# Kernel optimization log

Measured on AMD Instinct MI355X. Metric: run time of the kernel, lower is better.

Reference implementation:

```python
import jax, jax.numpy as jnp
import numpy as np

HIDDEN = 2048
N_HEADS = 16
HEAD_DIM = 128
N_EXPERTS = 8
TOP_K = 2
INTER = 1024
EPS = 1e-5
ROPE_THETA = 10000.0
T = 2048


def rms_norm(x, w, eps=EPS):
    xf = x.astype(jnp.float32)
    return (xf * jax.lax.rsqrt(jnp.mean(xf * xf, axis=-1, keepdims=True) + eps)).astype(x.dtype) * w


def apply_rope(x, positions):
    # x: [T, H, D], NeoX-style half rotation
    d = x.shape[-1]
    inv_freq = 1.0 / (ROPE_THETA ** (jnp.arange(0, d, 2, dtype=jnp.float32) / d))
    ang = positions.astype(jnp.float32)[:, None] * inv_freq  # [T, D/2]
    cos = jnp.cos(ang)[:, None, :]
    sin = jnp.sin(ang)[:, None, :]
    x1, x2 = jnp.split(x, 2, axis=-1)
    return jnp.concatenate([x1 * cos - x2 * sin, x2 * cos + x1 * sin], axis=-1)


def setup_inputs() -> dict:
    key = jax.random.key(0)
    ks = jax.random.split(key, 8)
    s = 0.02
    return {
        "positions": jnp.arange(T, dtype=jnp.int32),
        "hidden_states": jax.random.normal(ks[0], (T, HIDDEN), jnp.float32),
        "qkv_w": jax.random.normal(ks[1], (3 * HIDDEN, HIDDEN), jnp.float32) * s,
        "o_w": jax.random.normal(ks[2], (HIDDEN, HIDDEN), jnp.float32) * s,
        "q_norm_w": jnp.ones((N_HEADS * HEAD_DIM,), jnp.float32),
        "k_norm_w": jnp.ones((N_HEADS * HEAD_DIM,), jnp.float32),
        "post_attn_norm_w": jnp.ones((HIDDEN,), jnp.float32),
        "post_ffn_norm_w": jnp.ones((HIDDEN,), jnp.float32),
        "gate_w": jax.random.normal(ks[3], (N_EXPERTS, HIDDEN), jnp.float32) * s,
        "w_gate": jax.random.normal(ks[4], (N_EXPERTS, INTER, HIDDEN), jnp.float32) * s,
        "w_up": jax.random.normal(ks[5], (N_EXPERTS, INTER, HIDDEN), jnp.float32) * s,
        "w_down": jax.random.normal(ks[6], (N_EXPERTS, HIDDEN, INTER), jnp.float32) * s,
    }


def attention(positions, x, qkv_w, o_w, q_norm_w, k_norm_w):
    qkv = x @ qkv_w.T  # [T, 3*HIDDEN]
    q, k, v = jnp.split(qkv, 3, axis=-1)
    q = rms_norm(q, q_norm_w)  # norm over full flat q dim (FlexOlmo/OLMoE style)
    k = rms_norm(k, k_norm_w)
    q = apply_rope(q.reshape(T, N_HEADS, HEAD_DIM), positions)
    k = apply_rope(k.reshape(T, N_HEADS, HEAD_DIM), positions)
    v = v.reshape(T, N_HEADS, HEAD_DIM)
    scale = 1.0 / np.sqrt(HEAD_DIM)
    scores = jnp.einsum('thd,shd->hts', q, k) * scale
    mask = jnp.tril(jnp.ones((T, T), bool))
    scores = jnp.where(mask[None], scores, -jnp.inf)
    p = jax.nn.softmax(scores, axis=-1)
    out = jnp.einsum('hts,shd->thd', p, v).reshape(T, HIDDEN)
    return out @ o_w.T


def moe(x, gate_w, w_gate, w_up, w_down):
    logits = (x @ gate_w.T).astype(jnp.float32)  # router_logits.float()
    probs = jax.nn.softmax(logits, axis=-1)
    topv, topi = jax.lax.top_k(probs, TOP_K)  # renormalize=False -> use raw softmax weights
    # dense per-expert combine weights: [T, E]
    wdense = jnp.zeros((T, N_EXPERTS), jnp.float32)
    wdense = jnp.sum(jax.nn.one_hot(topi, N_EXPERTS, dtype=jnp.float32) * topv[..., None], axis=1)
    # detach().clone() before dispatch (inference semantics: value unchanged)
    xe = jax.lax.stop_gradient(x)
    g = jnp.einsum('td,efd->tef', xe, w_gate)
    u = jnp.einsum('td,efd->tef', xe, w_up)
    h = jax.nn.silu(g) * u
    y = jnp.einsum('tef,edf->ted', h, w_down)
    return jnp.einsum('ted,te->td', y, wdense)


def reference(positions, hidden_states, qkv_w, o_w, q_norm_w, k_norm_w,
              post_attn_norm_w, post_ffn_norm_w, gate_w, w_gate, w_up, w_down):
    residual = hidden_states
    h = attention(positions, hidden_states, qkv_w, o_w, q_norm_w, k_norm_w)
    h = rms_norm(h, post_attn_norm_w)
    h = h + residual
    residual = h
    h = moe(h, gate_w, w_gate, w_up, w_down)
    h = rms_norm(h, post_ffn_norm_w)
    return residual + h
```

## Files before the change

### kernel.cpp

```cpp
#include <hip/hip_runtime.h>
#include <hip/hip_bf16.h>
#include <cmath>

#define TT 2048
#define HID 2048
#define NHEADS 16
#define HDIM 128
#define NEXP 8
#define INTERD 1024
#define EPSV 1e-5f

typedef short bf16x8 __attribute__((ext_vector_type(8)));
typedef float f32x4 __attribute__((ext_vector_type(4)));

__device__ __forceinline__ unsigned short f2bf(float f) {
    unsigned int u = __builtin_bit_cast(unsigned int, f);
    unsigned int r = (u + 0x7FFFu + ((u >> 16) & 1u)) >> 16;
    return (unsigned short)r;
}
__device__ __forceinline__ float bf2f(unsigned short h) {
    return __builtin_bit_cast(float, (unsigned int)h << 16);
}

__device__ __forceinline__ void gll16(const void* g, void* l) {
    __builtin_amdgcn_global_load_lds((const __attribute__((address_space(1))) void*)g,
                                     (__attribute__((address_space(3))) void*)l, 16, 0, 0);
}

__device__ __forceinline__ float block_reduce_sum_256(float v, float* red) {
    const int tid = threadIdx.x;
    red[tid] = v;
    __syncthreads();
    for (int s = 128; s > 0; s >>= 1) {
        if (tid < s) red[tid] += red[tid + s];
        __syncthreads();
    }
    float r = red[0];
    __syncthreads();
    return r;
}

__global__ __launch_bounds__(256) void split_f32k(const float* __restrict__ x,
                                                  unsigned short* __restrict__ hi,
                                                  unsigned short* __restrict__ lo, int n4) {
    int i = blockIdx.x * 256 + threadIdx.x;
    if (i >= n4) return;
    float4 v = reinterpret_cast<const float4*>(x)[i];
    float xs[4] = {v.x, v.y, v.z, v.w};
    unsigned short hs[4], ls[4];
#pragma unroll
    for (int u = 0; u < 4; ++u) {
        hs[u] = f2bf(xs[u]);
        ls[u] = f2bf(xs[u] - bf2f(hs[u]));
    }
    uint2 hp; hp.x = hs[0] | ((unsigned)hs[1] << 16); hp.y = hs[2] | ((unsigned)hs[3] << 16);
    uint2 lp; lp.x = ls[0] | ((unsigned)ls[1] << 16); lp.y = ls[2] | ((unsigned)ls[3] << 16);
    *reinterpret_cast<uint2*>(hi + (size_t)i * 4) = hp;
    *reinterpret_cast<uint2*>(lo + (size_t)i * 4) = lp;
}

#define GSTAGE(BUF, K0)                                                             \
    {                                                                               \
        char* base_ = (char*)Smem + (BUF) * 32768;                                  \
        _Pragma("unroll")                                                           \
        for (int i_ = 0; i_ < 2; ++i_) {                                            \
            int c_ = tid + i_ * 256;                                                \
            int r_ = c_ >> 2, s_ = c_ & 3;                                          \
            int ko_ = (K0) + (((s_ ^ (r_ & 3)) & 3) << 3);                          \
            gll16(Ah + (size_t)(m0 + r_) * lda + ko_, base_ + c_ * 16);             \
            gll16(Al + (size_t)(m0 + r_) * lda + ko_, base_ + 8192 + c_ * 16);      \
            gll16(Bh + (size_t)(n0 + r_) * K + ko_, base_ + 16384 + c_ * 16);       \
            gll16(Bl + (size_t)(n0 + r_) * K + ko_, base_ + 24576 + c_ * 16);       \
        }                                                                           \
    }

__global__ __launch_bounds__(256) void gemm_sp(const unsigned short* __restrict__ Ah,
                                               const unsigned short* __restrict__ Al,
                                               const unsigned short* __restrict__ Bh,
                                               const unsigned short* __restrict__ Bl,
                                               float* __restrict__ C, int N, int K, int lda) {
    const int nbx = gridDim.x;
    const int nwg = nbx * gridDim.y;
    const int orig = blockIdx.y * nbx + blockIdx.x;
    const int qq = nwg >> 3, rr = nwg & 7;
    const int xcd = orig & 7, loc = orig >> 3;
    const int wgid = (xcd < rr ? xcd * (qq + 1) : rr * (qq + 1) + (xcd - rr) * qq) + loc;
    const int m0 = (wgid / nbx) * 128, n0 = (wgid % nbx) * 128;

    __shared__ __align__(16) unsigned short Smem[2 * 4 * 128 * 32];
    const int tid = threadIdx.x;
    const int w = tid >> 6, l = tid & 63;
    const int lr = l & 15, lg = l >> 4;
    const int wm = w >> 1, wn = w & 1;

    f32x4 acc[4][4];
#pragma unroll
    for (int i = 0; i < 4; ++i)
#pragma unroll
        for (int j = 0; j < 4; ++j) acc[i][j] = f32x4{0.f, 0.f, 0.f, 0.f};

    const int nks = K >> 5;
    GSTAGE(0, 0);
    int cur = 0;
    for (int ks = 0; ks < nks; ++ks) {
        if (ks + 1 < nks) {
            GSTAGE(cur ^ 1, (ks + 1) << 5);
            asm volatile("s_waitcnt vmcnt(8)" ::: "memory");
        } else {
            asm volatile("s_waitcnt vmcnt(0)" ::: "memory");
        }
        __builtin_amdgcn_s_barrier();
        __builtin_amdgcn_sched_barrier(0);
        char* bb = (char*)Smem + cur * 32768;
        bf16x8 bhf[4], blf[4];
#pragma unroll
        for (int nt = 0; nt < 4; ++nt) {
            int row = wn * 64 + nt * 16 + lr;
            int off = row * 64 + (((lg ^ (row & 3)) & 3) << 4);
            bhf[nt] = *reinterpret_cast<const bf16x8*>(bb + 16384 + off);
            blf[nt] = *reinterpret_cast<const bf16x8*>(bb + 24576 + off);
        }
        __builtin_amdgcn_s_setprio(1);
#pragma unroll
        for (int mt = 0; mt < 4; ++mt) {
            int row = wm * 64 + mt * 16 + lr;
            int off = row * 64 + (((lg ^ (row & 3)) & 3) << 4);
            bf16x8 ahf = *reinterpret_cast<const bf16x8*>(bb + off);
            bf16x8 alf = *reinterpret_cast<const bf16x8*>(bb + 8192 + off);
#pragma unroll
            for (int nt = 0; nt < 4; ++nt) {
                acc[mt][nt] = __builtin_amdgcn_mfma_f32_16x16x32_bf16(ahf, bhf[nt], acc[mt][nt], 0, 0, 0);
                acc[mt][nt] = __builtin_amdgcn_mfma_f32_16x16x32_bf16(ahf, blf[nt], acc[mt][nt], 0, 0, 0);
                acc[mt][nt] = __builtin_amdgcn_mfma_f32_16x16x32_bf16(alf, bhf[nt], acc[mt][nt], 0, 0, 0);
            }
        }
        __builtin_amdgcn_s_setprio(0);
        asm volatile("s_waitcnt lgkmcnt(0)" ::: "memory");
        __builtin_amdgcn_s_barrier();
        __builtin_amdgcn_sched_barrier(0);
        cur ^= 1;
    }
#pragma unroll
    for (int mt = 0; mt < 4; ++mt) {
#pragma unroll
        for (int r = 0; r < 4; ++r) {
            size_t crow = (size_t)(m0 + wm * 64 + mt * 16 + lg * 4 + r) * N;
#pragma unroll
            for (int nt = 0; nt < 4; ++nt)
                C[crow + n0 + wn * 64 + nt * 16 + lr] = acc[mt][nt][r];
        }
    }
}

template<int ABF, int MODE>
__global__ __launch_bounds__(256) void gemm_moe(const void* __restrict__ Ap,
                                                const float* __restrict__ B,
                                                float* __restrict__ C,
                                                const float* __restrict__ gsrc,
                                                int N, int K, int lda,
                                                size_t strideB,
                                                const int* __restrict__ gather,
                                                const int* __restrict__ offs,
                                                const int* __restrict__ counts) {
    const int e = blockIdx.z;
    const int cnt = counts[e];
    const int base = offs[e];
    const int m0 = blockIdx.y * 128;
    if (m0 >= cnt) return;
    const int n0 = blockIdx.x * 128;
    const float* Bp = B + (size_t)e * strideB;

    __shared__ unsigned short smA[128 * 64];
    __shared__ unsigned short smB[128 * 64];
    __shared__ int rowsA[128];
    const int tid = threadIdx.x;
    if (tid < 128) {
        int rr = min(m0 + tid, cnt - 1);
        rowsA[tid] = gather ? gather[base + rr] : (base + rr);
    }
    __syncthreads();

    const int w = tid >> 6, l = tid & 63;
    const int lr = l & 15, lg = l >> 4;
    const int wm = w >> 1, wn = w & 1;
    char* sA = (char*)smA;
    char* sB = (char*)smB;

    f32x4 acc[4][4];
#pragma unroll
    for (int i = 0; i < 4; ++i)
#pragma unroll
        for (int j = 0; j < 4; ++j) acc[i][j] = f32x4{0.f, 0.f, 0.f, 0.f};

    for (int k0 = 0; k0 < K; k0 += 64) {
        if (ABF) {
            const unsigned short* Abf = (const unsigned short*)Ap;
#pragma unroll
            for (int i = 0; i < 4; ++i) {
                int slot = tid + i * 256;
                int r = slot >> 3, sg = slot & 7;
                uint4 v = *reinterpret_cast<const uint4*>(&Abf[(size_t)rowsA[r] * lda + k0 + sg * 8]);
                *reinterpret_cast<uint4*>(sA + r * 128 + ((sg * 16) ^ ((r & 7) << 4))) = v;
            }
        } else {
            const float* Af = (const float*)Ap;
#pragma unroll
            for (int i = 0; i < 8; ++i) {
                int slot = tid + i * 256;
                int r = slot >> 4, kq = slot & 15;
                float4 av = *reinterpret_cast<const float4*>(&Af[(size_t)rowsA[r] * lda + k0 + kq * 4]);
                uint2 pk;
                pk.x = (unsigned)f2bf(av.x) | ((unsigned)f2bf(av.y) << 16);
                pk.y = (unsigned)f2bf(av.z) | ((unsigned)f2bf(av.w) << 16);
                *reinterpret_cast<uint2*>(sA + r * 128 + ((kq * 8) ^ ((r & 7) << 4))) = pk;
            }
        }
#pragma unroll
        for (int i = 0; i < 8; ++i) {
            int slot = tid + i * 256;
            int r = slot >> 4, kq = slot & 15;
            float4 bv = *reinterpret_cast<const float4*>(&Bp[(size_t)(n0 + r) * K + k0 + kq * 4]);
            uint2 pk;
            pk.x = (unsigned)f2bf(bv.x) | ((unsigned)f2bf(bv.y) << 16);
            pk.y = (unsigned)f2bf(bv.z) | ((unsigned)f2bf(bv.w) << 16);
            *reinterpret_cast<uint2*>(sB + r * 128 + ((kq * 8) ^ ((r & 7) << 4))) = pk;
        }
        __syncthreads();
#pragma unroll
        for (int kk = 0; kk < 2; ++kk) {
            bf16x8 af[4], bfr[4];
#pragma unroll
            for (int mt = 0; mt < 4; ++mt) {
                int row = wm * 64 + mt * 16 + lr;
                af[mt] = *reinterpret_cast<const bf16x8*>(sA + row * 128 + ((kk * 64 + lg * 16) ^ ((row & 7) << 4)));
            }
#pragma unroll
            for (int nt = 0; nt < 4; ++nt) {
                int row = wn * 64 + nt * 16 + lr;
                bfr[nt] = *reinterpret_cast<const bf16x8*>(sB + row * 128 + ((kk * 64 + lg * 16) ^ ((row & 7) << 4)));
            }
#pragma unroll
            for (int mt = 0; mt < 4; ++mt)
#pragma unroll
                for (int nt = 0; nt < 4; ++nt)
                    acc[mt][nt] = __builtin_amdgcn_mfma_f32_16x16x32_bf16(af[mt], bfr[nt], acc[mt][nt], 0, 0, 0);
        }
        __syncthreads();
    }
#pragma unroll
    for (int mt = 0; mt < 4; ++mt) {
#pragma unroll
        for (int r = 0; r < 4; ++r) {
            int rowl = wm * 64 + mt * 16 + lg * 4 + r;
            if (m0 + rowl < cnt) {
                size_t crow = (size_t)(base + m0 + rowl) * N;
#pragma unroll
                for (int nt = 0; nt < 4; ++nt) {
                    size_t idx = crow + n0 + wn * 64 + nt * 16 + lr;
                    if (MODE == 1) {
                        float g = gsrc[idx];
                        C[idx] = g / (1.f + expf(-g)) * acc[mt][nt][r];
                    } else {
                        C[idx] = acc[mt][nt][r];
                    }
                }
            }
        }
    }
}

__global__ __launch_bounds__(256) void qknorm_rope_split(float* __restrict__ qkv,
                                                         const float* __restrict__ qw,
                                                         const float* __restrict__ kw,
                                                         const int* __restrict__ pos) {
    __shared__ float xbuf[2048];
    __shared__ float red[256];
    const int t = blockIdx.x, tid = threadIdx.x;
    unsigned short* row16 = (unsigned short*)(qkv + (size_t)t * 6144);
    const float pf = (float)pos[t];
    float vreg[8];
    const float* vsrc = qkv + (size_t)t * 6144 + 4096;
#pragma unroll
    for (int i = 0; i < 8; ++i) vreg[i] = vsrc[tid + i * 256];
    __syncthreads();
#pragma unroll
    for (int i = 0; i < 8; ++i) {
        int d = tid + i * 256;
        unsigned short hi = f2bf(vreg[i]);
        row16[8192 + d] = hi;
        row16[10240 + d] = f2bf(vreg[i] - bf2f(hi));
    }
    for (int part = 0; part < 2; ++part) {
        const float* x = qkv + (size_t)t * 6144 + part * 2048;
        const float* wn = part ? kw : qw;
        const int sbase = part ? 4096 : 0;
        const float outscale = part ? 1.0f : 0.08838834764831845f;
        float s = 0.f;
#pragma unroll
        for (int i = 0; i < 8; ++i) {
            int d = tid + i * 256;
            float v = x[d];
            xbuf[d] = v;
            s = fmaf(v, v, s);
        }
        float tot = block_reduce_sum_256(s, red);
        float scale = rsqrtf(tot * (1.f / HID) + EPSV);
#pragma unroll
        for (int p = tid; p < 1024; p += 256) {
            int hh = p >> 6, j = p & 63;
            int i1 = hh * 128 + j, i2 = i1 + 64;
            float x1 = xbuf[i1] * scale * wn[i1];
            float x2 = xbuf[i2] * scale * wn[i2];
            float invf = expf(-(float)j * 0.14391156831212787f);
            float ang = pf * invf;
            float sn, cs;
            sincosf(ang, &sn, &cs);
            float o1 = (x1 * cs - x2 * sn) * outscale;
            float o2 = (x2 * cs + x1 * sn) * outscale;
            unsigned short h1_ = f2bf(o1);
            row16[sbase + i1] = h1_;
            row16[sbase + 2048 + i1] = f2bf(o1 - bf2f(h1_));
            unsigned short h2_ = f2bf(o2);
            row16[sbase + i2] = h2_;
            row16[sbase + 2048 + i2] = f2bf(o2 - bf2f(h2_));
        }
        __syncthreads();
    }
}

__global__ __launch_bounds__(256) void kvprep(const unsigned short* __restrict__ qkv16,
                                              unsigned short* __restrict__ kt,
                                              unsigned short* __restrict__ vt) {
    const int C = blockIdx.x;
    const int h = blockIdx.y;
    const int tid = threadIdx.x;
#pragma unroll
    for (int p = 0; p < 2; ++p) {
#pragma unroll
        for (int i = 0; i < 4; ++i) {
            int slot = tid + i * 256;
            int r = slot >> 4, sg = slot & 15;
            uint4 v = *reinterpret_cast<const uint4*>(
                qkv16 + (size_t)(C * 64 + r) * 12288 + 4096 + p * 2048 + h * 128 + (sg ^ (r & 7)) * 8);
            *reinterpret_cast<uint4*>(kt + (size_t)(h * 32 + C) * 16384 + p * 8192 + slot * 8) = v;
        }
    }
    __shared__ unsigned short tile[64 * 128];
    char* tb = (char*)tile;
    for (int p = 0; p < 2; ++p) {
#pragma unroll
        for (int i = 0; i < 4; ++i) {
            int c = tid + i * 256;
            int r = c >> 4, dseg = c & 15;
            uint4 v = *reinterpret_cast<const uint4*>(
                qkv16 + (size_t)(C * 64 + r) * 12288 + 8192 + p * 2048 + h * 128 + dseg * 8);
            int swz = dseg ^ (r & 7) ^ (r >> 3);
            *reinterpret_cast<uint4*>(tb + r * 256 + swz * 16) = v;
        }
        __syncthreads();
        unsigned short* ob = vt + (size_t)(h * 32 + C) * 16384 + p * 8192;
#pragma unroll
        for (int i = 0; i < 4; ++i) {
            int c = tid + i * 256;
            int d = c >> 3, j = c & 7;
            unsigned short tmp[8];
#pragma unroll
            for (int u = 0; u < 8; ++u) {
                int s = 8 * j + u;
                int swz = (d >> 3) ^ (s & 7) ^ (s >> 3);
                tmp[u] = *reinterpret_cast<const unsigned short*>(tb + s * 256 + swz * 16 + (d & 7) * 2);
            }
            *reinterpret_cast<uint4*>(ob + (size_t)d * 64 + ((j ^ (d & 7)) * 8)) =
                *reinterpret_cast<const uint4*>(tmp);
        }
        __syncthreads();
    }
}

#define STAGE1(CIDX)                                                                   \
    {                                                                                  \
        const unsigned short* kb_ = kt + (size_t)(h * 32 + (CIDX)) * 16384;            \
        const unsigned short* vb_ = vt + (size_t)(h * 32 + (CIDX)) * 16384;            \
        _Pragma("unroll")                                                              \
        for (int p_ = 0; p_ < 2; ++p_) {                                               \
            _Pragma("unroll")                                                          \
            for (int i_ = 0; i_ < 4; ++i_) {                                           \
                int slot_ = tid + i_ * 256;                                            \
                gll16(kb_ + p_ * 8192 + slot_ * 8, kvb + p_ * 16384 + slot_ * 16);     \
                gll16(vb_ + p_ * 8192 + slot_ * 8, kvb + 32768 + p_ * 16384 + slot_ * 16); \
            }                                                                          \
        }                                                                              \
    }

__global__ __launch_bounds__(256) void attn_mfma(const unsigned short* __restrict__ qkv16,
                                                 const unsigned short* __restrict__ kt,
                                                 const unsigned short* __restrict__ vt,
                                                 unsigned short* __restrict__ oh,
                                                 unsigned short* __restrict__ ol) {
    const int g = blockIdx.x;
    const int rank = (g < 256) ? g : 767 - g;
    const int h = rank & 15;
    const int t0 = (31 - (rank >> 4)) * 64;
    const int tid = threadIdx.x;
    const int w = tid >> 6, l = tid & 63;
    const int lr = l & 15, lg = l >> 4;
    const size_t RS = 12288;
    __shared__ __align__(16) unsigned short KVs[32768];
    __shared__ unsigned short Ps[4][2 * 16 * 64];
    char* kvb = (char*)KVs;
    char* PsB = (char*)(Ps[w]);

    bf16x8 qh[4], ql[4];
    {
        const unsigned short* qp = qkv16 + (size_t)(t0 + w * 16 + lr) * RS + h * 128 + lg * 8;
#pragma unroll
        for (int kk = 0; kk < 4; ++kk) {
            qh[kk] = *reinterpret_cast<const bf16x8*>(qp + kk * 32);
            ql[kk] = *reinterpret_cast<const bf16x8*>(qp + 2048 + kk * 32);
        }
    }
    f32x4 oacc[8];
#pragma unroll
    for (int dt = 0; dt < 8; ++dt) oacc[dt] = f32x4{0.f, 0.f, 0.f, 0.f};
    float mrun[4] = {-INFINITY, -INFINITY, -INFINITY, -INFINITY};
    float lrun[4] = {0.f, 0.f, 0.f, 0.f};

    for (int s0 = 0; s0 <= t0; s0 += 64) {
        STAGE1(s0 >> 6);
        __syncthreads();
        char* KsB = kvb;
        char* VtB = kvb + 32768;

        f32x4 sc[4];
#pragma unroll
        for (int nt = 0; nt < 4; ++nt) sc[nt] = f32x4{0.f, 0.f, 0.f, 0.f};
        __builtin_amdgcn_s_setprio(1);
#pragma unroll
        for (int kk = 0; kk < 4; ++kk) {
#pragma unroll
            for (int nt = 0; nt < 4; ++nt) {
                int row = nt * 16 + lr;
                int off = row * 256 + ((kk * 64 + lg * 16) ^ ((row & 7) << 4));
                bf16x8 kh = *reinterpret_cast<const bf16x8*>(KsB + off);
                bf16x8 kl = *reinterpret_cast<const bf16x8*>(KsB + 16384 + off);
                sc[nt] = __builtin_amdgcn_mfma_f32_16x16x32_bf16(qh[kk], kh, sc[nt], 0, 0, 0);
                sc[nt] = __builtin_amdgcn_mfma_f32_16x16x32_bf16(ql[kk], kh, sc[nt], 0, 0, 0);
                sc[nt] = __builtin_amdgcn_mfma_f32_16x16x32_bf16(qh[kk], kl, sc[nt], 0, 0, 0);
            }
        }
        __builtin_amdgcn_s_setprio(0);
        float mnew[4], alpha[4], psum[4];
#pragma unroll
        for (int r = 0; r < 4; ++r) {
            int row_t = t0 + w * 16 + lg * 4 + r;
            float mx = mrun[r];
#pragma unroll
            for (int nt = 0; nt < 4; ++nt) {
                int col = s0 + nt * 16 + lr;
                float v = sc[nt][r];
                if (col > row_t) v = -INFINITY;
                sc[nt][r] = v;
                mx = fmaxf(mx, v);
            }
#pragma unroll
            for (int o = 1; o < 16; o <<= 1) mx = fmaxf(mx, __shfl_xor(mx, o));
            mnew[r] = mx;
            alpha[r] = expf(mrun[r] - mx);
            mrun[r] = mx;
            psum[r] = 0.f;
        }
#pragma unroll
        for (int nt = 0; nt < 4; ++nt) {
#pragma unroll
            for (int r = 0; r < 4; ++r) {
                float p = expf(sc[nt][r] - mnew[r]);
                psum[r] += p;
                int prow = lg * 4 + r;
                int off = prow * 128 + (((nt * 16 + lr) * 2) ^ ((prow & 7) << 4));
                unsigned short ph = f2bf(p);
                *reinterpret_cast<unsigned short*>(PsB + off) = ph;
                *reinterpret_cast<unsigned short*>(PsB + 2048 + off) = f2bf(p - bf2f(ph));
            }
        }
#pragma unroll
        for (int r = 0; r < 4; ++r) {
            float s = psum[r];
#pragma unroll
            for (int o = 1; o < 16; o <<= 1) s += __shfl_xor(s, o);
            lrun[r] = lrun[r] * alpha[r] + s;
        }
#pragma unroll
        for (int dt = 0; dt < 8; ++dt)
#pragma unroll
            for (int r = 0; r < 4; ++r) oacc[dt][r] *= alpha[r];
        bf16x8 ph[2], pl[2];
#pragma unroll
        for (int kk = 0; kk < 2; ++kk) {
            int off = lr * 128 + ((kk * 64 + lg * 16) ^ ((lr & 7) << 4));
            ph[kk] = *reinterpret_cast<const bf16x8*>(PsB + off);
            pl[kk] = *reinterpret_cast<const bf16x8*>(PsB + 2048 + off);
        }
        __builtin_amdgcn_s_setprio(1);
#pragma unroll
        for (int dt = 0; dt < 8; ++dt) {
            int row = dt * 16 + lr;
#pragma unroll
            for (int kk = 0; kk < 2; ++kk) {
                int off = row * 128 + ((kk * 64 + lg * 16) ^ ((row & 7) << 4));
                bf16x8 vh = *reinterpret_cast<const bf16x8*>(VtB + off);
                bf16x8 vl = *reinterpret_cast<const bf16x8*>(VtB + 16384 + off);
                oacc[dt] = __builtin_amdgcn_mfma_f32_16x16x32_bf16(ph[kk], vh, oacc[dt], 0, 0, 0);
                oacc[dt] = __builtin_amdgcn_mfma_f32_16x16x32_bf16(ph[kk], vl, oacc[dt], 0, 0, 0);
                oacc[dt] = __builtin_amdgcn_mfma_f32_16x16x32_bf16(pl[kk], vh, oacc[dt], 0, 0, 0);
            }
        }
        __builtin_amdgcn_s_setprio(0);
        __syncthreads();
    }
#pragma unroll
    for (int r = 0; r < 4; ++r) {
        float inv = 1.f / lrun[r];
        int row_t = t0 + w * 16 + lg * 4 + r;
#pragma unroll
        for (int dt = 0; dt < 8; ++dt) {
            float o = oacc[dt][r] * inv;
            unsigned short hb = f2bf(o);
            size_t idx = (size_t)row_t * 2048 + h * 128 + dt * 16 + lr;
            oh[idx] = hb;
            ol[idx] = f2bf(o - bf2f(hb));
        }
    }
}

__global__ __launch_bounds__(256) void add_rmsnorm(const float* __restrict__ resid,
                                                   const float* __restrict__ x,
                                                   const float* __restrict__ w,
                                                   float* __restrict__ out,
                                                   unsigned short* __restrict__ outbf) {
    __shared__ float red[256];
    const int t = blockIdx.x, tid = threadIdx.x;
    const float* xr = x + (size_t)t * HID;
    float v[8];
    float s = 0.f;
#pragma unroll
    for (int i = 0; i < 8; ++i) { v[i] = xr[tid + i * 256]; s = fmaf(v[i], v[i], s); }
    float tot = block_reduce_sum_256(s, red);
    float scale = rsqrtf(tot * (1.f / HID) + EPSV);
#pragma unroll
    for (int i = 0; i < 8; ++i) {
        int d = tid + i * 256;
        float o = resid[(size_t)t * HID + d] + v[i] * scale * w[d];
        out[(size_t)t * HID + d] = o;
        outbf[(size_t)t * HID + d] = f2bf(o);
    }
}

__global__ __launch_bounds__(64) void router_kernel(const float* __restrict__ h1,
                                                    const float* __restrict__ gate_w,
                                                    int* __restrict__ topi, float* __restrict__ topv,
                                                    int* __restrict__ slot_tk, int* __restrict__ counts) {
    const int t = blockIdx.x, lane = threadIdx.x;
    float acc[NEXP] = {};
    const float* x = h1 + (size_t)t * HID;
    for (int d = lane; d < HID; d += 64) {
        float xv = x[d];
#pragma unroll
        for (int e = 0; e < NEXP; ++e) acc[e] = fmaf(xv, gate_w[e * HID + d], acc[e]);
    }
#pragma unroll
    for (int e = 0; e < NEXP; ++e)
#pragma unroll
        for (int off = 32; off > 0; off >>= 1) acc[e] += __shfl_down(acc[e], off);
    if (lane == 0) {
        float mx = acc[0];
        for (int e = 1; e < NEXP; ++e) mx = fmaxf(mx, acc[e]);
        float p[NEXP], se = 0.f;
        for (int e = 0; e < NEXP; ++e) { p[e] = expf(acc[e] - mx); se += p[e]; }
        float inv = 1.f / se;
        for (int e = 0; e < NEXP; ++e) p[e] *= inv;
        int e1 = 0;
        for (int e = 1; e < NEXP; ++e) if (p[e] > p[e1]) e1 = e;
        int e2 = (e1 == 0) ? 1 : 0;
        for (int e = 0; e < NEXP; ++e) if (e != e1 && p[e] > p[e2]) e2 = e;
        topi[t * 2] = e1;     topv[t * 2] = p[e1];
        topi[t * 2 + 1] = e2; topv[t * 2 + 1] = p[e2];
        slot_tk[t * 2]     = atomicAdd(&counts[e1], 1);
        slot_tk[t * 2 + 1] = atomicAdd(&counts[e2], 1);
    }
}

__global__ void scan_kernel(const int* __restrict__ counts, int* __restrict__ offs) {
    int o = 0;
    for (int e = 0; e < NEXP; ++e) { offs[e] = o; o += counts[e]; }
}

__global__ __launch_bounds__(256) void map_kernel(const int* __restrict__ topi,
                                                  const int* __restrict__ slot_tk,
                                                  const int* __restrict__ offs,
                                                  int* __restrict__ token_of_row,
                                                  int* __restrict__ row_of_tk) {
    int idx = blockIdx.x * 256 + threadIdx.x;
    if (idx >= TT * 2) return;
    int e = topi[idx];
    int row = offs[e] + slot_tk[idx];
    token_of_row[row] = idx >> 1;
    row_of_tk[idx] = row;
}

__global__ __launch_bounds__(256) void final_combine(const float* __restrict__ h1,
                                                     const float* __restrict__ ypart,
                                                     const float* __restrict__ topv,
                                                     const int* __restrict__ row_of_tk,
                                                     const float* __restrict__ wffn,
                                                     float* __restrict__ out) {
    __shared__ float red[256];
    const int t = blockIdx.x, tid = threadIdx.x;
    const int r0 = row_of_tk[t * 2], r1 = row_of_tk[t * 2 + 1];
    const float w0 = topv[t * 2], w1 = topv[t * 2 + 1];
    const float* y0 = ypart + (size_t)r0 * HID;
    const float* y1 = ypart + (size_t)r1 * HID;
    float v[8];
    float s = 0.f;
#pragma unroll
    for (int i = 0; i < 8; ++i) {
        int d = tid + i * 256;
        v[i] = w0 * y0[d] + w1 * y1[d];
        s = fmaf(v[i], v[i], s);
    }
    float tot = block_reduce_sum_256(s, red);
    float scale = rsqrtf(tot * (1.f / HID) + EPSV);
#pragma unroll
    for (int i = 0; i < 8; ++i) {
        int d = tid + i * 256;
        out[(size_t)t * HID + d] = h1[(size_t)t * HID + d] + v[i] * scale * wffn[d];
    }
}

extern "C" void kernel_launch(void* const* d_in, const int* in_sizes, int n_in,
                              void* d_out, int out_size, void* d_ws, size_t ws_size,
                              hipStream_t stream) {
    const int*   positions = (const int*)d_in[0];
    const float* hidden    = (const float*)d_in[1];
    const float* qkv_w     = (const float*)d_in[2];
    const float* o_w       = (const float*)d_in[3];
    const float* q_norm_w  = (const float*)d_in[4];
    const float* k_norm_w  = (const float*)d_in[5];
    const float* post_attn = (const float*)d_in[6];
    const float* post_ffn  = (const float*)d_in[7];
    const float* gate_w    = (const float*)d_in[8];
    const float* w_gate    = (const float*)d_in[9];
    const float* w_up      = (const float*)d_in[10];
    const float* w_down    = (const float*)d_in[11];
    float* out = (float*)d_out;

    char* ws = (char*)d_ws;
    size_t off = 0;
    auto alloc = [&](size_t bytes) -> void* {
        void* p = ws + off;
        off += (bytes + 255) & ~(size_t)255;
        return p;
    };
    float*          qkvbuf = (float*)alloc((size_t)TT * 6144 * 4);
    unsigned short* hidsp  = (unsigned short*)alloc((size_t)TT * HID * 2 * 2);
    unsigned short* wsp    = (unsigned short*)alloc(((size_t)6144 * HID * 2 + (size_t)HID * HID * 2) * 2);
    float*          h1     = (float*)alloc((size_t)TT * HID * 4);
    unsigned short* h1bf   = (unsigned short*)alloc((size_t)TT * HID * 2);
    int*   topi   = (int*)alloc(TT * 2 * 4);
    float* topv   = (float*)alloc(TT * 2 * 4);
    int*   slot   = (int*)alloc(TT * 2 * 4);
    int*   rowtk  = (int*)alloc(TT * 2 * 4);
    int*   tokrow = (int*)alloc(TT * 2 * 4);
    int*   counts = (int*)alloc(8 * 4);
    int*   offsb  = (int*)alloc(8 * 4);
    if (off > ws_size) return;

    unsigned short* hid_hi   = hidsp;
    unsigned short* hid_lo   = hidsp + (size_t)TT * HID;
    unsigned short* attnO_hi = hid_hi;
    unsigned short* attnO_lo = hid_lo;
    unsigned short* qkvw_hi = wsp;
    unsigned short* qkvw_lo = wsp + (size_t)6144 * HID;
    unsigned short* ow_hi   = wsp + (size_t)2 * 6144 * HID;
    unsigned short* ow_lo   = ow_hi + (size_t)HID * HID;
    unsigned short* vtbuf   = wsp;
    unsigned short* ktbuf   = wsp + (size_t)TT * HID * 2;
    float* gbuf   = qkvbuf;
    float* hinter = qkvbuf + (size_t)4096 * INTERD;
    float* oOut   = qkvbuf + (size_t)8192 * INTERD;
    float* ypart  = oOut;

    hipMemsetAsync(counts, 0, 8 * sizeof(int), stream);

    dim3 b256(256);
    split_f32k<<<dim3(TT * HID / 4 / 256), b256, 0, stream>>>(hidden, hid_hi, hid_lo, TT * HID / 4);
    split_f32k<<<dim3(6144 * HID / 4 / 256), b256, 0, stream>>>(qkv_w, qkvw_hi, qkvw_lo, 6144 * HID / 4);
    split_f32k<<<dim3(HID * HID / 4 / 256), b256, 0, stream>>>(o_w, ow_hi, ow_lo, HID * HID / 4);
    gemm_sp<<<dim3(6144 / 128, TT / 128), b256, 0, stream>>>(hid_hi, hid_lo, qkvw_hi, qkvw_lo,
                                                             qkvbuf, 6144, HID, HID);
    qknorm_rope_split<<<dim3(TT), b256, 0, stream>>>(qkvbuf, q_norm_w, k_norm_w, positions);
    kvprep<<<dim3(32, NHEADS), b256, 0, stream>>>((const unsigned short*)qkvbuf, ktbuf, vtbuf);
    attn_mfma<<<dim3(512), b256, 0, stream>>>((const unsigned short*)qkvbuf, ktbuf, vtbuf,
                                              attnO_hi, attnO_lo);
    gemm_sp<<<dim3(HID / 128, TT / 128), b256, 0, stream>>>(attnO_hi, attnO_lo, ow_hi, ow_lo,
                                                            oOut, HID, HID, HID);
    add_rmsnorm<<<dim3(TT), b256, 0, stream>>>(hidden, oOut, post_attn, h1, h1bf);
    router_kernel<<<dim3(TT), dim3(64), 0, stream>>>(h1, gate_w, topi, topv, slot, counts);
    scan_kernel<<<1, 1, 0, stream>>>(counts, offsb);
    map_kernel<<<dim3((TT * 2 + 255) / 256), b256, 0, stream>>>(topi, slot, offsb, tokrow, rowtk);
    gemm_moe<1, 0><<<dim3(INTERD / 128, 32, NEXP), b256, 0, stream>>>(
        h1bf, w_gate, gbuf, nullptr, INTERD, HID, HID, (size_t)INTERD * HID, tokrow, offsb, counts);
    gemm_moe<1, 1><<<dim3(INTERD / 128, 32, NEXP), b256, 0, stream>>>(
        h1bf, w_up, hinter, gbuf, INTERD, HID, HID, (size_t)INTERD * HID, tokrow, offsb, counts);
    gemm_moe<0, 0><<<dim3(HID / 128, 32, NEXP), b256, 0, stream>>>(
        hinter, w_down, ypart, nullptr, HID, INTERD, INTERD, (size_t)HID * INTERD, nullptr, offsb, counts);
    final_combine<<<dim3(TT), b256, 0, stream>>>(h1, ypart, topv, rowtk, post_ffn, out);
}
```

Baseline: 696.7 us.

## Pre-convert MoE gate/up weights to bf16 and use async-LDS pipelined expert GEMM

Adds a conversion kernel that turns the fp32 w_gate and w_up expert weights into bf16 buffers in the workspace. The gate and up GEMMs then use a new double-buffered kernel with direct global-to-LDS loads, instead of converting fp32 B tiles inside the loop. The up GEMM now writes the SiLU-gated intermediate as bf16, so the down GEMM reads bf16 A directly. The LDS swizzle also changes to XOR with (row>>1)&3 to reduce bank conflicts. The risk is the extra weight-conversion traffic on every call, plus lower precision in the intermediate.

```diff
diff --git a/kernel.cpp b/kernel.cpp
--- a/kernel.cpp
+++ b/kernel.cpp
@@ -59,6 +59,17 @@
     *reinterpret_cast<uint2*>(lo + (size_t)i * 4) = lp;
 }
 
+__global__ __launch_bounds__(256) void cvt_bf(const float* __restrict__ x,
+                                              unsigned short* __restrict__ y, int n4) {
+    int i = blockIdx.x * 256 + threadIdx.x;
+    if (i >= n4) return;
+    float4 v = reinterpret_cast<const float4*>(x)[i];
+    uint2 p;
+    p.x = (unsigned)f2bf(v.x) | ((unsigned)f2bf(v.y) << 16);
+    p.y = (unsigned)f2bf(v.z) | ((unsigned)f2bf(v.w) << 16);
+    *reinterpret_cast<uint2*>(y + (size_t)i * 4) = p;
+}
+
 #define GSTAGE(BUF, K0)                                                             \
     {                                                                               \
         char* base_ = (char*)Smem + (BUF) * 32768;                                  \
@@ -66,7 +77,7 @@
         for (int i_ = 0; i_ < 2; ++i_) {                                            \
             int c_ = tid + i_ * 256;                                                \
             int r_ = c_ >> 2, s_ = c_ & 3;                                          \
-            int ko_ = (K0) + (((s_ ^ (r_ & 3)) & 3) << 3);                          \
+            int ko_ = (K0) + (((s_ ^ ((r_ >> 1) & 3)) & 3) << 3);                   \
             gll16(Ah + (size_t)(m0 + r_) * lda + ko_, base_ + c_ * 16);             \
             gll16(Al + (size_t)(m0 + r_) * lda + ko_, base_ + 8192 + c_ * 16);      \
             gll16(Bh + (size_t)(n0 + r_) * K + ko_, base_ + 16384 + c_ * 16);       \
@@ -116,7 +127,7 @@
 #pragma unroll
         for (int nt = 0; nt < 4; ++nt) {
             int row = wn * 64 + nt * 16 + lr;
-            int off = row * 64 + (((lg ^ (row & 3)) & 3) << 4);
+            int off = row * 64 + (((lg ^ ((row >> 1) & 3)) & 3) << 4);
             bhf[nt] = *reinterpret_cast<const bf16x8*>(bb + 16384 + off);
             blf[nt] = *reinterpret_cast<const bf16x8*>(bb + 24576 + off);
         }
@@ -124,7 +135,7 @@
 #pragma unroll
         for (int mt = 0; mt < 4; ++mt) {
             int row = wm * 64 + mt * 16 + lr;
-            int off = row * 64 + (((lg ^ (row & 3)) & 3) << 4);
+            int off = row * 64 + (((lg ^ ((row >> 1) & 3)) & 3) << 4);
             bf16x8 ahf = *reinterpret_cast<const bf16x8*>(bb + off);
             bf16x8 alf = *reinterpret_cast<const bf16x8*>(bb + 8192 + off);
 #pragma unroll
@@ -152,16 +163,120 @@
     }
 }
 
-template<int ABF, int MODE>
-__global__ __launch_bounds__(256) void gemm_moe(const void* __restrict__ Ap,
-                                                const float* __restrict__ B,
-                                                float* __restrict__ C,
-                                                const float* __restrict__ gsrc,
-                                                int N, int K, int lda,
-                                                size_t strideB,
-                                                const int* __restrict__ gather,
-                                                const int* __restrict__ offs,
-                                                const int* __restrict__ counts) {
+#define GSTAGE_BF(BUF, K0)                                                           \
+    {                                                                                \
+        char* base_ = sm + (BUF) * 16384;                                            \
+        int ko_ = (K0) + x0s;                                                        \
+        gll16(A + arow0 * lda + ko_, base_ + tid * 16);                              \
+        gll16(A + arow1 * lda + ko_, base_ + (tid + 256) * 16);                      \
+        gll16(Bp + brow0 * K + ko_, base_ + 8192 + tid * 16);                        \
+        gll16(Bp + brow1 * K + ko_, base_ + 8192 + (tid + 256) * 16);                \
+    }
+
+template<int MODE>
+__global__ __launch_bounds__(256) void gemm_bf(const unsigned short* __restrict__ A,
+                                               const unsigned short* __restrict__ B,
+                                               void* __restrict__ Cout,
+                                               const float* __restrict__ gsrc,
+                                               int N, int K, int lda,
+                                               size_t strideB,
+                                               const int* __restrict__ gather,
+                                               const int* __restrict__ offs,
+                                               const int* __restrict__ counts) {
+    const int e = blockIdx.z;
+    const int cnt = counts[e];
+    const int base = offs[e];
+    const int m0 = blockIdx.y * 128;
+    if (m0 >= cnt) return;
+    const int n0 = blockIdx.x * 128;
+    const unsigned short* Bp = B + (size_t)e * strideB;
+
+    __shared__ __align__(16) unsigned short Smem[2 * 2 * 128 * 32];
+    char* sm = (char*)Smem;
+    const int tid = threadIdx.x;
+    const int w = tid >> 6, l = tid & 63;
+    const int lr = l & 15, lg = l >> 4;
+    const int wm = w >> 1, wn = w & 1;
+
+    const int r0 = tid >> 2, s0 = tid & 3;
+    const int r1 = r0 + 64;
+    const int x0s = ((s0 ^ ((r0 >> 1) & 3)) & 3) << 3;
+    const size_t arow0 = (size_t)gather[base + min(m0 + r0, cnt - 1)];
+    const size_t arow1 = (size_t)gather[base + min(m0 + r1, cnt - 1)];
+    const size_t brow0 = (size_t)(n0 + r0);
+    const size_t brow1 = (size_t)(n0 + r1);
+
+    f32x4 acc[4][4];
+#pragma unroll
+    for (int i = 0; i < 4; ++i)
+#pragma unroll
+        for (int j = 0; j < 4; ++j) acc[i][j] = f32x4{0.f, 0.f, 0.f, 0.f};
+
+    const int nks = K >> 5;
+    GSTAGE_BF(0, 0);
+    int cur = 0;
+    for (int ks = 0; ks < nks; ++ks) {
+        if (ks + 1 < nks) {
+            GSTAGE_BF(cur ^ 1, (ks + 1) << 5);
+            asm volatile("s_waitcnt vmcnt(4)" ::: "memory");
+        } else {
+            asm volatile("s_waitcnt vmcnt(0)" ::: "memory");
+        }
+        __builtin_amdgcn_s_barrier();
+        __builtin_amdgcn_sched_barrier(0);
+        char* bb = sm + cur * 16384;
+        bf16x8 bfr[4];
+#pragma unroll
+        for (int nt = 0; nt < 4; ++nt) {
+            int row = wn * 64 + nt * 16 + lr;
+            int off = row * 64 + (((lg ^ ((row >> 1) & 3)) & 3) << 4);
+            bfr[nt] = *reinterpret_cast<const bf16x8*>(bb + 8192 + off);
+        }
+        __builtin_amdgcn_s_setprio(1);
+#pragma unroll
+        for (int mt = 0; mt < 4; ++mt) {
+            int row = wm * 64 + mt * 16 + lr;
+            int off = row * 64 + (((lg ^ ((row >> 1) & 3)) & 3) << 4);
+            bf16x8 af = *reinterpret_cast<const bf16x8*>(bb + off);
+#pragma unroll
+            for (int nt = 0; nt < 4; ++nt)
+                acc[mt][nt] = __builtin_amdgcn_mfma_f32_16x16x32_bf16(af, bfr[nt], acc[mt][nt], 0, 0, 0);
+        }
+        __builtin_amdgcn_s_setprio(0);
+        asm volatile("s_waitcnt lgkmcnt(0)" ::: "memory");
+        __builtin_amdgcn_s_barrier();
+        __builtin_amdgcn_sched_barrier(0);
+        cur ^= 1;
+    }
+#pragma unroll
+    for (int mt = 0; mt < 4; ++mt) {
+#pragma unroll
+        for (int r = 0; r < 4; ++r) {
+            int rowl = wm * 64 + mt * 16 + lg * 4 + r;
+            if (m0 + rowl < cnt) {
+                size_t crow = (size_t)(base + m0 + rowl) * N;
+#pragma unroll
+                for (int nt = 0; nt < 4; ++nt) {
+                    size_t idx = crow + n0 + wn * 64 + nt * 16 + lr;
+                    if (MODE == 1) {
+                        float g = gsrc[idx];
+                        ((unsigned short*)Cout)[idx] = f2bf(g / (1.f + expf(-g)) * acc[mt][nt][r]);
+                    } else {
+                        ((float*)Cout)[idx] = acc[mt][nt][r];
+                    }
+                }
+            }
+        }
+    }
+}
+
+__global__ __launch_bounds__(256) void gemm_moe_down(const unsigned short* __restrict__ Abf,
+                                                     const float* __restrict__ B,
+                                                     float* __restrict__ C,
+                                                     int N, int K, int lda,
+                                                     size_t strideB,
+                                                     const int* __restrict__ offs,
+                                                     const int* __restrict__ counts) {
     const int e = blockIdx.z;
     const int cnt = counts[e];
     const int base = offs[e];
@@ -172,14 +287,7 @@
 
     __shared__ unsigned short smA[128 * 64];
     __shared__ unsigned short smB[128 * 64];
-    __shared__ int rowsA[128];
     const int tid = threadIdx.x;
-    if (tid < 128) {
-        int rr = min(m0 + tid, cnt - 1);
-        rowsA[tid] = gather ? gather[base + rr] : (base + rr);
-    }
-    __syncthreads();
-
     const int w = tid >> 6, l = tid & 63;
     const int lr = l & 15, lg = l >> 4;
     const int wm = w >> 1, wn = w & 1;
@@ -193,27 +301,13 @@
         for (int j = 0; j < 4; ++j) acc[i][j] = f32x4{0.f, 0.f, 0.f, 0.f};
 
     for (int k0 = 0; k0 < K; k0 += 64) {
-        if (ABF) {
-            const unsigned short* Abf = (const unsigned short*)Ap;
-#pragma unroll
-            for (int i = 0; i < 4; ++i) {
-                int slot = tid + i * 256;
-                int r = slot >> 3, sg = slot & 7;
-                uint4 v = *reinterpret_cast<const uint4*>(&Abf[(size_t)rowsA[r] * lda + k0 + sg * 8]);
-                *reinterpret_cast<uint4*>(sA + r * 128 + ((sg * 16) ^ ((r & 7) << 4))) = v;
-            }
-        } else {
-            const float* Af = (const float*)Ap;
-#pragma unroll
-            for (int i = 0; i < 8; ++i) {
-                int slot = tid + i * 256;
-                int r = slot >> 4, kq = slot & 15;
-                float4 av = *reinterpret_cast<const float4*>(&Af[(size_t)rowsA[r] * lda + k0 + kq * 4]);
-                uint2 pk;
-                pk.x = (unsigned)f2bf(av.x) | ((unsigned)f2bf(av.y) << 16);
-                pk.y = (unsigned)f2bf(av.z) | ((unsigned)f2bf(av.w) << 16);
-                *reinterpret_cast<uint2*>(sA + r * 128 + ((kq * 8) ^ ((r & 7) << 4))) = pk;
-            }
+#pragma unroll
+        for (int i = 0; i < 4; ++i) {
+            int slot = tid + i * 256;
+            int r = slot >> 3, sg = slot & 7;
+            int arow = base + min(m0 + r, cnt - 1);
+            uint4 v = *reinterpret_cast<const uint4*>(&Abf[(size_t)arow * lda + k0 + sg * 8]);
+            *reinterpret_cast<uint4*>(sA + r * 128 + ((sg * 16) ^ ((r & 7) << 4))) = v;
         }
 #pragma unroll
         for (int i = 0; i < 8; ++i) {
@@ -255,15 +349,8 @@
             if (m0 + rowl < cnt) {
                 size_t crow = (size_t)(base + m0 + rowl) * N;
 #pragma unroll
-                for (int nt = 0; nt < 4; ++nt) {
-                    size_t idx = crow + n0 + wn * 64 + nt * 16 + lr;
-                    if (MODE == 1) {
-                        float g = gsrc[idx];
-                        C[idx] = g / (1.f + expf(-g)) * acc[mt][nt][r];
-                    } else {
-                        C[idx] = acc[mt][nt][r];
-                    }
-                }
+                for (int nt = 0; nt < 4; ++nt)
+                    C[crow + n0 + wn * 64 + nt * 16 + lr] = acc[mt][nt][r];
             }
         }
     }
@@ -684,10 +771,12 @@
     unsigned short* ow_lo   = ow_hi + (size_t)HID * HID;
     unsigned short* vtbuf   = wsp;
     unsigned short* ktbuf   = wsp + (size_t)TT * HID * 2;
-    float* gbuf   = qkvbuf;
-    float* hinter = qkvbuf + (size_t)4096 * INTERD;
-    float* oOut   = qkvbuf + (size_t)8192 * INTERD;
-    float* ypart  = oOut;
+    unsigned short* wbfg = wsp;
+    unsigned short* wbfu = wsp + (size_t)NEXP * INTERD * HID;
+    float*          gbuf   = qkvbuf;
+    unsigned short* hinter = (unsigned short*)(qkvbuf + (size_t)4096 * INTERD);
+    float*          oOut   = qkvbuf + (size_t)8192 * INTERD;
+    float*          ypart  = oOut;
 
     hipMemsetAsync(counts, 0, 8 * sizeof(int), stream);
 
@@ -703,15 +792,17 @@
                                               attnO_hi, attnO_lo);
     gemm_sp<<<dim3(HID / 128, TT / 128), b256, 0, stream>>>(attnO_hi, attnO_lo, ow_hi, ow_lo,
                                                             oOut, HID, HID, HID);
+    cvt_bf<<<dim3(16384), b256, 0, stream>>>(w_gate, wbfg, NEXP * INTERD * HID / 4);
+    cvt_bf<<<dim3(16384), b256, 0, stream>>>(w_up,   wbfu, NEXP * INTERD * HID / 4);
     add_rmsnorm<<<dim3(TT), b256, 0, stream>>>(hidden, oOut, post_attn, h1, h1bf);
     router_kernel<<<dim3(TT), dim3(64), 0, stream>>>(h1, gate_w, topi, topv, slot, counts);
     scan_kernel<<<1, 1, 0, stream>>>(counts, offsb);
     map_kernel<<<dim3((TT * 2 + 255) / 256), b256, 0, stream>>>(topi, slot, offsb, tokrow, rowtk);
-    gemm_moe<1, 0><<<dim3(INTERD / 128, 32, NEXP), b256, 0, stream>>>(
-        h1bf, w_gate, gbuf, nullptr, INTERD, HID, HID, (size_t)INTERD * HID, tokrow, offsb, counts);
-    gemm_moe<1, 1><<<dim3(INTERD / 128, 32, NEXP), b256, 0, stream>>>(
-        h1bf, w_up, hinter, gbuf, INTERD, HID, HID, (size_t)INTERD * HID, tokrow, offsb, counts);
-    gemm_moe<0, 0><<<dim3(HID / 128, 32, NEXP), b256, 0, stream>>>(
-        hinter, w_down, ypart, nullptr, HID, INTERD, INTERD, (size_t)HID * INTERD, nullptr, offsb, counts);
+    gemm_bf<0><<<dim3(INTERD / 128, 32, NEXP), b256, 0, stream>>>(
+        h1bf, wbfg, gbuf, nullptr, INTERD, HID, HID, (size_t)INTERD * HID, tokrow, offsb, counts);
+    gemm_bf<1><<<dim3(INTERD / 128, 32, NEXP), b256, 0, stream>>>(
+        h1bf, wbfu, hinter, gbuf, INTERD, HID, HID, (size_t)INTERD * HID, tokrow, offsb, counts);
+    gemm_moe_down<<<dim3(HID / 128, 32, NEXP), b256, 0, stream>>>(
+        hinter, w_down, ypart, HID, INTERD, INTERD, (size_t)HID * INTERD, offsb, counts);
     final_combine<<<dim3(TT), b256, 0, stream>>>(h1, ypart, topv, rowtk, post_ffn, out);
 }
```

New measurement: 717.7 us (median of 2 runs). 3.0% more time.
